# Performance work log

Measured on AMD Instinct MI355X. Metric: run time of the kernel, lower is better.

## Reference

```python
import jax, jax.numpy as jnp
import numpy as np

B, S, IN_F, OUT_F = 8, 2048, 2048, 2048
ORDER, RANK, LEAF = 3, 4, 13  # LEAF = ceil(IN_F ** (1/ORDER))


def setup_inputs() -> dict:
    key = jax.random.key(0)
    k1, k2, k3, k4 = jax.random.split(key, 4)
    inp = jax.random.normal(k1, (B, S, IN_F), dtype=jnp.float32)
    # leaf init ~ uniform(-std, std), std = gain / in_features**(1/order)
    gain = float(np.sqrt(2.0 / (1.0 + 5.0)))  # leaky_relu gain with param=sqrt(5)
    std = gain / (IN_F ** (1.0 / ORDER))
    leaf_tensor = jax.random.uniform(k2, (ORDER, RANK, LEAF, LEAF), dtype=jnp.float32,
                                     minval=-std, maxval=std)
    bound = 1.0 / np.sqrt(IN_F)
    weight = jax.random.uniform(k3, (OUT_F, IN_F), dtype=jnp.float32, minval=-bound, maxval=bound)
    bias = jax.random.uniform(k4, (OUT_F,), dtype=jnp.float32, minval=-bound, maxval=bound)
    return {"input": inp, "leaf_tensor": leaf_tensor, "weight": weight, "bias": bias}


def tensor_product_represent(leaf_tensor, out_dim, in_dim):
    order, rank, leaf, _ = leaf_tensor.shape  # static shapes
    base = leaf_tensor[0]                      # [rank, leaf, leaf]
    dim = leaf
    for i in range(1, order):                  # fixed small structural loop
        # Kronecker step: [r, d, d] x [r, l, l] -> [r, d*l, d*l]
        base = jnp.einsum('abc,ade->abdce', base, leaf_tensor[i])
        dim = dim * leaf
        base = base.reshape(rank, dim, dim)
    base = base.sum(axis=0)                    # [leaf^order, leaf^order]
    return base[:out_dim, :in_dim]


def reference(input, leaf_tensor, weight, bias):
    out_dim, in_dim = weight.shape
    delta = tensor_product_represent(leaf_tensor, out_dim, in_dim)
    w = weight + delta                          # [out, in]
    # F.linear: y = x @ w.T + b
    return jnp.einsum('bsi,oi->bso', input, w) + bias
```

## Files before the change

### kernel.cpp

```cpp
#include <hip/hip_runtime.h>
#include <hip/hip_bf16.h>
#include <stdint.h>

#define MROWS 16384
#define KDIM  2048
#define NDIM  2048
#define LEAFD 13
#define RANKD 4

typedef __bf16 bf16x8 __attribute__((ext_vector_type(8)));
typedef float  f32x4  __attribute__((ext_vector_type(4)));

__global__ void build_w_kernel(const float* __restrict__ weight,
                               const float* __restrict__ leaf,
                               __hip_bfloat16* __restrict__ wbf) {
    __shared__ float ll[3 * RANKD * LEAFD * LEAFD];
    for (int t = threadIdx.x; t < 3 * RANKD * LEAFD * LEAFD; t += blockDim.x)
        ll[t] = leaf[t];
    __syncthreads();
    int idx = blockIdx.x * blockDim.x + threadIdx.x;
    if (idx >= NDIM * KDIM) return;
    int o = idx / KDIM, i = idx % KDIM;
    int o2 = o / 169, o1 = (o / 13) % 13, o0 = o % 13;
    int i2 = i / 169, i1 = (i / 13) % 13, i0 = i % 13;
    float d = 0.f;
#pragma unroll
    for (int r = 0; r < RANKD; ++r) {
        float a = ll[( r            * LEAFD + o2) * LEAFD + i2];
        float b = ll[((RANKD   + r) * LEAFD + o1) * LEAFD + i1];
        float c = ll[((2*RANKD + r) * LEAFD + o0) * LEAFD + i0];
        d += a * b * c;
    }
    wbf[idx] = __float2bfloat16(weight[idx] + d);
}

__global__ void cvt_kernel(const float* __restrict__ x,
                           __hip_bfloat16* __restrict__ xb, int n) {
    long stride = (long)gridDim.x * blockDim.x * 4;
    for (long idx = ((long)blockIdx.x * blockDim.x + threadIdx.x) * 4; idx < n; idx += stride) {
        float4 v = *reinterpret_cast<const float4*>(x + idx);
        __hip_bfloat16 tmp[4];
        tmp[0] = __float2bfloat16(v.x);
        tmp[1] = __float2bfloat16(v.y);
        tmp[2] = __float2bfloat16(v.z);
        tmp[3] = __float2bfloat16(v.w);
        *reinterpret_cast<uint2*>(xb + idx) = *reinterpret_cast<const uint2*>(tmp);
    }
}

#define BM 128
#define BN 128
#define BK 32

__device__ __forceinline__ void gload_lds16(const void* g, void* l) {
    __builtin_amdgcn_global_load_lds((const __attribute__((address_space(1))) void*)g,
                                     (__attribute__((address_space(3))) void*)l,
                                     16, 0, 0);
}

__global__ __launch_bounds__(256) void gemm_kernel(const __hip_bfloat16* __restrict__ A,
                                                   const __hip_bfloat16* __restrict__ Wb,
                                                   const float* __restrict__ bias,
                                                   float* __restrict__ C) {
    __shared__ __hip_bfloat16 sA[BM * BK];
    __shared__ __hip_bfloat16 sB[BN * BK];

    const int bid  = blockIdx.x;
    const int bn   = bid & 15;
    const int bm   = bid >> 4;
    const int tid  = threadIdx.x;
    const int lane = tid & 63;
    const int wid  = tid >> 6;
    const int wr   = wid >> 1;
    const int wc   = wid & 1;

    const size_t arow0 = (size_t)bm * BM;
    const size_t brow0 = (size_t)bn * BN;

    f32x4 acc[4][4];
#pragma unroll
    for (int m = 0; m < 4; ++m)
#pragma unroll
        for (int n = 0; n < 4; ++n)
            acc[m][n] = (f32x4){0.f, 0.f, 0.f, 0.f};

    const int rsel = lane & 15;
    const int ksel = (lane >> 4) * 8;

    for (int kt = 0; kt < KDIM / BK; ++kt) {
        const int k0 = kt * BK;
#pragma unroll
        for (int j = 0; j < 2; ++j) {
            const int c   = (wid * 2 + j) * 64 + lane;
            const int row = c >> 2;
            const int ch  = c & 3;
            const __hip_bfloat16* ga = A  + (arow0 + row) * KDIM + k0 + ch * 8;
            const __hip_bfloat16* gb = Wb + (brow0 + row) * KDIM + k0 + ch * 8;
            gload_lds16(ga, &sA[(wid * 2 + j) * 512]);
            gload_lds16(gb, &sB[(wid * 2 + j) * 512]);
        }
        __syncthreads();

        bf16x8 af[4], bfr[4];
#pragma unroll
        for (int m = 0; m < 4; ++m)
            af[m] = *reinterpret_cast<const bf16x8*>(&sA[(wr * 64 + m * 16 + rsel) * BK + ksel]);
#pragma unroll
        for (int n = 0; n < 4; ++n)
            bfr[n] = *reinterpret_cast<const bf16x8*>(&sB[(wc * 64 + n * 16 + rsel) * BK + ksel]);

#pragma unroll
        for (int m = 0; m < 4; ++m)
#pragma unroll
            for (int n = 0; n < 4; ++n)
                acc[m][n] = __builtin_amdgcn_mfma_f32_16x16x32_bf16(af[m], bfr[n], acc[m][n], 0, 0, 0);

        __syncthreads();
    }

    const int col0 = lane & 15;
    const int r0   = (lane >> 4) * 4;
#pragma unroll
    for (int n = 0; n < 4; ++n) {
        const int cg = bn * BN + wc * 64 + n * 16 + col0;
        const float bv = bias[cg];
#pragma unroll
        for (int m = 0; m < 4; ++m) {
            const size_t rg = arow0 + wr * 64 + m * 16 + r0;
#pragma unroll
            for (int r = 0; r < 4; ++r)
                C[(rg + r) * NDIM + cg] = acc[m][n][r] + bv;
        }
    }
}

__global__ void naive_kernel(const float* __restrict__ x,
                             const float* __restrict__ leaf,
                             const float* __restrict__ W,
                             const float* __restrict__ bias,
                             float* __restrict__ out) {
    long idx = (long)blockIdx.x * blockDim.x + threadIdx.x;
    if (idx >= (long)MROWS * NDIM) return;
    int  o = (int)(idx % NDIM);
    long m = idx / NDIM;
    int o2 = o / 169, o1 = (o / 13) % 13, o0 = o % 13;
    float acc = 0.f;
    for (int i = 0; i < KDIM; ++i) {
        int i2 = i / 169, i1 = (i / 13) % 13, i0 = i % 13;
        float d = 0.f;
#pragma unroll
        for (int r = 0; r < RANKD; ++r)
            d += leaf[( r     * LEAFD + o2) * LEAFD + i2]
               * leaf[((4 + r) * LEAFD + o1) * LEAFD + i1]
               * leaf[((8 + r) * LEAFD + o0) * LEAFD + i0];
        acc += x[m * KDIM + i] * (W[(long)o * KDIM + i] + d);
    }
    out[idx] = acc + bias[o];
}

extern "C" void kernel_launch(void* const* d_in, const int* in_sizes, int n_in,
                              void* d_out, int out_size, void* d_ws, size_t ws_size,
                              hipStream_t stream) {
    const float* x      = (const float*)d_in[0];
    const float* leaf   = (const float*)d_in[1];
    const float* weight = (const float*)d_in[2];
    const float* bias   = (const float*)d_in[3];
    float* out = (float*)d_out;

    const size_t needA = (size_t)MROWS * KDIM * sizeof(__hip_bfloat16);
    const size_t needW = (size_t)NDIM  * KDIM * sizeof(__hip_bfloat16);

    if (ws_size >= needA + needW) {
        __hip_bfloat16* xb = (__hip_bfloat16*)d_ws;
        __hip_bfloat16* wb = (__hip_bfloat16*)((char*)d_ws + needA);
        build_w_kernel<<<(NDIM * KDIM + 255) / 256, 256, 0, stream>>>(weight, leaf, wb);
        cvt_kernel<<<2048, 256, 0, stream>>>(x, xb, MROWS * KDIM);
        gemm_kernel<<<(MROWS / BM) * (NDIM / BN), 256, 0, stream>>>(xb, wb, bias, out);
    } else {
        long total = (long)MROWS * NDIM;
        naive_kernel<<<(int)((total + 255) / 256), 256, 0, stream>>>(x, leaf, weight, bias, out);
    }
}
```

Measured before the change: 248.4 us.

## Replace GEMM with 256x256 double-buffered 8-wave kernel with swizzled LDS

Rewrites the bf16 GEMM to use 256x256 block tiles with 512 threads, a K-step of 64 split into two 32-wide halves, and double-buffered LDS fed by global_load_lds, so the next tile's loads overlap the current MFMAs. LDS addresses are XOR-swizzled to avoid bank conflicts, and block IDs are remapped for better L2 locality. A hand-built schedule of barriers, waitcnts and setprio interleaves the loads with MFMA quarters. The goal is to raise arithmetic intensity and hide memory latency, at the cost of higher register and LDS pressure and a fragile manual schedule.

```diff
diff --git a/kernel.cpp b/kernel.cpp
--- a/kernel.cpp
+++ b/kernel.cpp
@@ -48,85 +48,168 @@
     }
 }
 
-#define BM 128
-#define BN 128
-#define BK 32
-
-__device__ __forceinline__ void gload_lds16(const void* g, void* l) {
+
+__device__ __forceinline__ void gload16(const __hip_bfloat16* g, char* l) {
     __builtin_amdgcn_global_load_lds((const __attribute__((address_space(1))) void*)g,
                                      (__attribute__((address_space(3))) void*)l,
                                      16, 0, 0);
 }
 
-__global__ __launch_bounds__(256) void gemm_kernel(const __hip_bfloat16* __restrict__ A,
-                                                   const __hip_bfloat16* __restrict__ Wb,
-                                                   const float* __restrict__ bias,
-                                                   float* __restrict__ C) {
-    __shared__ __hip_bfloat16 sA[BM * BK];
-    __shared__ __hip_bfloat16 sB[BN * BK];
-
-    const int bid  = blockIdx.x;
-    const int bn   = bid & 15;
-    const int bm   = bid >> 4;
+#define STAGE(base, kb, bufi, slot) do {                                          \
+    gload16((base) + (kb) + gOff0, smemc + (bufi)*65536 + (slot)*16384 + lOff0);  \
+    gload16((base) + (kb) + gOff1, smemc + (bufi)*65536 + (slot)*16384 + lOff1);  \
+} while (0)
+
+#define LOAD_A(mh, kk, bufc)                                                        \
+    af0 = *(const bf16x8*)(smemc + (bufc)*65536 + (kk)*32768 + offA[(mh)*4+0]);     \
+    af1 = *(const bf16x8*)(smemc + (bufc)*65536 + (kk)*32768 + offA[(mh)*4+1]);     \
+    af2 = *(const bf16x8*)(smemc + (bufc)*65536 + (kk)*32768 + offA[(mh)*4+2]);     \
+    af3 = *(const bf16x8*)(smemc + (bufc)*65536 + (kk)*32768 + offA[(mh)*4+3]);
+
+#define LOAD_B(kk, bufc)                                                                    \
+    bf0 = *(const bf16x8*)(smemc + (bufc)*65536 + (kk)*32768 + 16384 + offB[0]);            \
+    bf1 = *(const bf16x8*)(smemc + (bufc)*65536 + (kk)*32768 + 16384 + offB[1]);            \
+    bf2 = *(const bf16x8*)(smemc + (bufc)*65536 + (kk)*32768 + 16384 + offB[2]);            \
+    bf3 = *(const bf16x8*)(smemc + (bufc)*65536 + (kk)*32768 + 16384 + offB[3]);
+
+#define MFMA_Q(mh) do {                                                                   \
+    acc[(mh)*4+0][0] = __builtin_amdgcn_mfma_f32_16x16x32_bf16(af0, bf0, acc[(mh)*4+0][0], 0,0,0); \
+    acc[(mh)*4+1][0] = __builtin_amdgcn_mfma_f32_16x16x32_bf16(af1, bf0, acc[(mh)*4+1][0], 0,0,0); \
+    acc[(mh)*4+2][0] = __builtin_amdgcn_mfma_f32_16x16x32_bf16(af2, bf0, acc[(mh)*4+2][0], 0,0,0); \
+    acc[(mh)*4+3][0] = __builtin_amdgcn_mfma_f32_16x16x32_bf16(af3, bf0, acc[(mh)*4+3][0], 0,0,0); \
+    acc[(mh)*4+0][1] = __builtin_amdgcn_mfma_f32_16x16x32_bf16(af0, bf1, acc[(mh)*4+0][1], 0,0,0); \
+    acc[(mh)*4+1][1] = __builtin_amdgcn_mfma_f32_16x16x32_bf16(af1, bf1, acc[(mh)*4+1][1], 0,0,0); \
+    acc[(mh)*4+2][1] = __builtin_amdgcn_mfma_f32_16x16x32_bf16(af2, bf1, acc[(mh)*4+2][1], 0,0,0); \
+    acc[(mh)*4+3][1] = __builtin_amdgcn_mfma_f32_16x16x32_bf16(af3, bf1, acc[(mh)*4+3][1], 0,0,0); \
+    acc[(mh)*4+0][2] = __builtin_amdgcn_mfma_f32_16x16x32_bf16(af0, bf2, acc[(mh)*4+0][2], 0,0,0); \
+    acc[(mh)*4+1][2] = __builtin_amdgcn_mfma_f32_16x16x32_bf16(af1, bf2, acc[(mh)*4+1][2], 0,0,0); \
+    acc[(mh)*4+2][2] = __builtin_amdgcn_mfma_f32_16x16x32_bf16(af2, bf2, acc[(mh)*4+2][2], 0,0,0); \
+    acc[(mh)*4+3][2] = __builtin_amdgcn_mfma_f32_16x16x32_bf16(af3, bf2, acc[(mh)*4+3][2], 0,0,0); \
+    acc[(mh)*4+0][3] = __builtin_amdgcn_mfma_f32_16x16x32_bf16(af0, bf3, acc[(mh)*4+0][3], 0,0,0); \
+    acc[(mh)*4+1][3] = __builtin_amdgcn_mfma_f32_16x16x32_bf16(af1, bf3, acc[(mh)*4+1][3], 0,0,0); \
+    acc[(mh)*4+2][3] = __builtin_amdgcn_mfma_f32_16x16x32_bf16(af2, bf3, acc[(mh)*4+2][3], 0,0,0); \
+    acc[(mh)*4+3][3] = __builtin_amdgcn_mfma_f32_16x16x32_bf16(af3, bf3, acc[(mh)*4+3][3], 0,0,0); \
+} while (0)
+
+#define BARRIER_IN do {                                     \
+    __builtin_amdgcn_sched_barrier(0);                      \
+    __builtin_amdgcn_s_barrier();                           \
+    asm volatile("s_waitcnt lgkmcnt(0)" ::: "memory");      \
+    __builtin_amdgcn_sched_barrier(0);                      \
+    __builtin_amdgcn_s_setprio(1);                          \
+} while (0)
+
+#define BARRIER_OUT do {                                    \
+    __builtin_amdgcn_s_setprio(0);                          \
+    __builtin_amdgcn_sched_barrier(0);                      \
+    __builtin_amdgcn_s_barrier();                           \
+    __builtin_amdgcn_sched_barrier(0);                      \
+} while (0)
+
+#define WAIT4 asm volatile("s_waitcnt vmcnt(4)" ::: "memory")
+#define WAIT0 asm volatile("s_waitcnt vmcnt(0)" ::: "memory")
+#define WNONE do {} while (0)
+
+#define KTILE(t, bufc, S0, S1, S2, S3, W3) do {                     \
+                                                  \
+    LOAD_B(0, bufc); LOAD_A(0, 0, bufc);                            \
+    if (S0) STAGE(Abase, ((t)+1)*64+32, (bufc)^1, 2);               \
+    BARRIER_IN; MFMA_Q(0); BARRIER_OUT;                             \
+                                                  \
+    LOAD_A(1, 0, bufc);                                             \
+    if (S1) STAGE(Bbase, ((t)+1)*64+32, (bufc)^1, 3);               \
+    BARRIER_IN; MFMA_Q(1); BARRIER_OUT;                             \
+                                                  \
+    LOAD_B(1, bufc); LOAD_A(0, 1, bufc);                            \
+    if (S2) STAGE(Abase, ((t)+2)*64, (bufc), 0);                    \
+    BARRIER_IN; MFMA_Q(0); BARRIER_OUT;                             \
+                                                  \
+    LOAD_A(1, 1, bufc);                                             \
+    if (S3) STAGE(Bbase, ((t)+2)*64, (bufc), 1);                    \
+    W3;                                                             \
+    BARRIER_IN; MFMA_Q(1); BARRIER_OUT;                             \
+} while (0)
+
+__global__ __launch_bounds__(512, 2) void gemm8_kernel(const __hip_bfloat16* __restrict__ A,
+                                                       const __hip_bfloat16* __restrict__ Wb,
+                                                       const float* __restrict__ bias,
+                                                       float* __restrict__ C) {
+    __shared__ __align__(16) __hip_bfloat16 smem[2][4][8192];
+    char* smemc = (char*)&smem[0][0][0];
+
     const int tid  = threadIdx.x;
     const int lane = tid & 63;
     const int wid  = tid >> 6;
-    const int wr   = wid >> 1;
-    const int wc   = wid & 1;
-
-    const size_t arow0 = (size_t)bm * BM;
-    const size_t brow0 = (size_t)bn * BN;
-
-    f32x4 acc[4][4];
-#pragma unroll
-    for (int m = 0; m < 4; ++m)
+    const int wr   = wid >> 2;
+    const int wc   = wid & 3;
+
+    const int bid = blockIdx.x;
+    const int swz = (bid & 7) * 64 + (bid >> 3);
+    const int bn  = swz >> 6;
+    const int bm  = swz & 63;
+
+    const __hip_bfloat16* Abase = A  + (size_t)bm * 256 * KDIM;
+    const __hip_bfloat16* Bbase = Wb + (size_t)bn * 256 * KDIM;
+
+    const int c0  = wid * 64 + lane;
+    const int c1  = 512 + wid * 64 + lane;
+    const int cs0 = c0 ^ ((c0 >> 3) & 7);
+    const int cs1 = c1 ^ ((c1 >> 3) & 7);
+    const int gOff0 = (cs0 >> 2) * KDIM + (cs0 & 3) * 8;
+    const int gOff1 = (cs1 >> 2) * KDIM + (cs1 & 3) * 8;
+    const int lOff0 = wid * 1024;
+    const int lOff1 = 8192 + wid * 1024;
+
+    const int rsel = lane & 15;
+    const int kby  = (lane >> 4) * 16;
+    int offA[8], offB[4];
+#pragma unroll
+    for (int m = 0; m < 8; ++m) {
+        int a = (wr * 128 + m * 16 + rsel) * 64 + kby;
+        offA[m] = a ^ (((a >> 7) & 7) << 4);
+    }
+#pragma unroll
+    for (int n = 0; n < 4; ++n) {
+        int a = (wc * 64 + n * 16 + rsel) * 64 + kby;
+        offB[n] = a ^ (((a >> 7) & 7) << 4);
+    }
+
+    f32x4 acc[8][4];
+#pragma unroll
+    for (int m = 0; m < 8; ++m)
 #pragma unroll
         for (int n = 0; n < 4; ++n)
             acc[m][n] = (f32x4){0.f, 0.f, 0.f, 0.f};
 
-    const int rsel = lane & 15;
-    const int ksel = (lane >> 4) * 8;
-
-    for (int kt = 0; kt < KDIM / BK; ++kt) {
-        const int k0 = kt * BK;
-#pragma unroll
-        for (int j = 0; j < 2; ++j) {
-            const int c   = (wid * 2 + j) * 64 + lane;
-            const int row = c >> 2;
-            const int ch  = c & 3;
-            const __hip_bfloat16* ga = A  + (arow0 + row) * KDIM + k0 + ch * 8;
-            const __hip_bfloat16* gb = Wb + (brow0 + row) * KDIM + k0 + ch * 8;
-            gload_lds16(ga, &sA[(wid * 2 + j) * 512]);
-            gload_lds16(gb, &sB[(wid * 2 + j) * 512]);
-        }
-        __syncthreads();
-
-        bf16x8 af[4], bfr[4];
-#pragma unroll
-        for (int m = 0; m < 4; ++m)
-            af[m] = *reinterpret_cast<const bf16x8*>(&sA[(wr * 64 + m * 16 + rsel) * BK + ksel]);
-#pragma unroll
-        for (int n = 0; n < 4; ++n)
-            bfr[n] = *reinterpret_cast<const bf16x8*>(&sB[(wc * 64 + n * 16 + rsel) * BK + ksel]);
-
-#pragma unroll
-        for (int m = 0; m < 4; ++m)
-#pragma unroll
-            for (int n = 0; n < 4; ++n)
-                acc[m][n] = __builtin_amdgcn_mfma_f32_16x16x32_bf16(af[m], bfr[n], acc[m][n], 0, 0, 0);
-
-        __syncthreads();
-    }
+    bf16x8 af0, af1, af2, af3, bf0, bf1, bf2, bf3;
+
+    STAGE(Abase,  0, 0, 0);
+    STAGE(Bbase,  0, 0, 1);
+    STAGE(Abase, 32, 0, 2);
+    STAGE(Bbase, 32, 0, 3);
+    STAGE(Abase, 64, 1, 0);
+    STAGE(Bbase, 64, 1, 1);
+    WAIT4;
+    __builtin_amdgcn_sched_barrier(0);
+    __builtin_amdgcn_s_barrier();
+    __builtin_amdgcn_sched_barrier(0);
+
+    for (int tt = 0; tt < 30; tt += 2) {
+        KTILE(tt,     0, 1, 1, 1, 1, WAIT4);
+        KTILE(tt + 1, 1, 1, 1, 1, 1, WAIT4);
+    }
+    KTILE(30, 0, 1, 1, 0, 0, WAIT0);
+    KTILE(31, 1, 0, 0, 0, 0, WNONE);
 
     const int col0 = lane & 15;
     const int r0   = (lane >> 4) * 4;
 #pragma unroll
     for (int n = 0; n < 4; ++n) {
-        const int cg = bn * BN + wc * 64 + n * 16 + col0;
+        const int cg = bn * 256 + wc * 64 + n * 16 + col0;
         const float bv = bias[cg];
 #pragma unroll
-        for (int m = 0; m < 4; ++m) {
-            const size_t rg = arow0 + wr * 64 + m * 16 + r0;
+        for (int m = 0; m < 8; ++m) {
+            const size_t rg = (size_t)bm * 256 + wr * 128 + m * 16 + r0;
 #pragma unroll
             for (int r = 0; r < 4; ++r)
                 C[(rg + r) * NDIM + cg] = acc[m][n][r] + bv;
@@ -175,7 +258,7 @@
         __hip_bfloat16* wb = (__hip_bfloat16*)((char*)d_ws + needA);
         build_w_kernel<<<(NDIM * KDIM + 255) / 256, 256, 0, stream>>>(weight, leaf, wb);
         cvt_kernel<<<2048, 256, 0, stream>>>(x, xb, MROWS * KDIM);
-        gemm_kernel<<<(MROWS / BM) * (NDIM / BN), 256, 0, stream>>>(xb, wb, bias, out);
+        gemm8_kernel<<<(MROWS / 256) * (NDIM / 256), 512, 0, stream>>>(xb, wb, bias, out);
     } else {
         long total = (long)MROWS * NDIM;
         naive_kernel<<<(int)((total + 255) / 256), 256, 0, stream>>>(x, leaf, weight, bias, out);
```

Result: faster. 208.3 us (-16.1%).

## Rewrite GEMM with triple-buffered LDS pipeline, XOR swizzle, and 128x256 tiles

Applied to the files above, without the earlier changes.

Replaces the single-buffered 128x128 GEMM with a 512-thread 128x256-tile kernel. It uses a three-stage global_load_lds ring with explicit vmcnt waits and a single barrier per k-step, XOR-swizzled LDS addressing to avoid bank conflicts, and a block-index swizzle for L2 reuse. It also raises MFMA priority via s_setprio and widens the fp32-to-bf16 conversion to 8 elements per thread. This aims to hide load latency and remove the double-syncthreads stalls, at the cost of more LDS per block and fragile hand-tuned waitcnt logic.

```diff
diff --git a/kernel.cpp b/kernel.cpp
--- a/kernel.cpp
+++ b/kernel.cpp
@@ -36,46 +36,127 @@
 
 __global__ void cvt_kernel(const float* __restrict__ x,
                            __hip_bfloat16* __restrict__ xb, int n) {
-    long stride = (long)gridDim.x * blockDim.x * 4;
-    for (long idx = ((long)blockIdx.x * blockDim.x + threadIdx.x) * 4; idx < n; idx += stride) {
-        float4 v = *reinterpret_cast<const float4*>(x + idx);
-        __hip_bfloat16 tmp[4];
-        tmp[0] = __float2bfloat16(v.x);
-        tmp[1] = __float2bfloat16(v.y);
-        tmp[2] = __float2bfloat16(v.z);
-        tmp[3] = __float2bfloat16(v.w);
-        *reinterpret_cast<uint2*>(xb + idx) = *reinterpret_cast<const uint2*>(tmp);
-    }
-}
-
-#define BM 128
-#define BN 128
-#define BK 32
-
-__device__ __forceinline__ void gload_lds16(const void* g, void* l) {
+    long stride = (long)gridDim.x * blockDim.x * 8;
+    for (long idx = ((long)blockIdx.x * blockDim.x + threadIdx.x) * 8; idx < n; idx += stride) {
+        float4 v0 = *reinterpret_cast<const float4*>(x + idx);
+        float4 v1 = *reinterpret_cast<const float4*>(x + idx + 4);
+        __hip_bfloat16 tmp[8];
+        tmp[0] = __float2bfloat16(v0.x); tmp[1] = __float2bfloat16(v0.y);
+        tmp[2] = __float2bfloat16(v0.z); tmp[3] = __float2bfloat16(v0.w);
+        tmp[4] = __float2bfloat16(v1.x); tmp[5] = __float2bfloat16(v1.y);
+        tmp[6] = __float2bfloat16(v1.z); tmp[7] = __float2bfloat16(v1.w);
+        *reinterpret_cast<uint4*>(xb + idx) = *reinterpret_cast<const uint4*>(tmp);
+    }
+}
+
+
+__device__ __forceinline__ void gload16(const __hip_bfloat16* g, char* l) {
     __builtin_amdgcn_global_load_lds((const __attribute__((address_space(1))) void*)g,
                                      (__attribute__((address_space(3))) void*)l,
                                      16, 0, 0);
 }
 
-__global__ __launch_bounds__(256) void gemm_kernel(const __hip_bfloat16* __restrict__ A,
-                                                   const __hip_bfloat16* __restrict__ Wb,
-                                                   const float* __restrict__ bias,
-                                                   float* __restrict__ C) {
-    __shared__ __hip_bfloat16 sA[BM * BK];
-    __shared__ __hip_bfloat16 sB[BN * BK];
-
-    const int bid  = blockIdx.x;
-    const int bn   = bid & 15;
-    const int bm   = bid >> 4;
+#define RD(off) (*(const bf16x8*)(smemc + (off)))
+
+#define MFMA16 do {                                                                 \
+    acc[0][0] = __builtin_amdgcn_mfma_f32_16x16x32_bf16(af0, bf0, acc[0][0],0,0,0); \
+    acc[1][0] = __builtin_amdgcn_mfma_f32_16x16x32_bf16(af1, bf0, acc[1][0],0,0,0); \
+    acc[2][0] = __builtin_amdgcn_mfma_f32_16x16x32_bf16(af2, bf0, acc[2][0],0,0,0); \
+    acc[3][0] = __builtin_amdgcn_mfma_f32_16x16x32_bf16(af3, bf0, acc[3][0],0,0,0); \
+    acc[0][1] = __builtin_amdgcn_mfma_f32_16x16x32_bf16(af0, bf1, acc[0][1],0,0,0); \
+    acc[1][1] = __builtin_amdgcn_mfma_f32_16x16x32_bf16(af1, bf1, acc[1][1],0,0,0); \
+    acc[2][1] = __builtin_amdgcn_mfma_f32_16x16x32_bf16(af2, bf1, acc[2][1],0,0,0); \
+    acc[3][1] = __builtin_amdgcn_mfma_f32_16x16x32_bf16(af3, bf1, acc[3][1],0,0,0); \
+    acc[0][2] = __builtin_amdgcn_mfma_f32_16x16x32_bf16(af0, bf2, acc[0][2],0,0,0); \
+    acc[1][2] = __builtin_amdgcn_mfma_f32_16x16x32_bf16(af1, bf2, acc[1][2],0,0,0); \
+    acc[2][2] = __builtin_amdgcn_mfma_f32_16x16x32_bf16(af2, bf2, acc[2][2],0,0,0); \
+    acc[3][2] = __builtin_amdgcn_mfma_f32_16x16x32_bf16(af3, bf2, acc[3][2],0,0,0); \
+    acc[0][3] = __builtin_amdgcn_mfma_f32_16x16x32_bf16(af0, bf3, acc[0][3],0,0,0); \
+    acc[1][3] = __builtin_amdgcn_mfma_f32_16x16x32_bf16(af1, bf3, acc[1][3],0,0,0); \
+    acc[2][3] = __builtin_amdgcn_mfma_f32_16x16x32_bf16(af2, bf3, acc[2][3],0,0,0); \
+    acc[3][3] = __builtin_amdgcn_mfma_f32_16x16x32_bf16(af3, bf3, acc[3][3],0,0,0); \
+} while (0)
+
+#define W3 asm volatile("s_waitcnt vmcnt(3)" ::: "memory")
+#define W0 asm volatile("s_waitcnt vmcnt(0)" ::: "memory")
+
+#define KT(t, BC, BS, SG, WT) do {                                              \
+    af0 = RD((BC)*24576 + offA0);                                               \
+    af1 = RD((BC)*24576 + offA0 + 1024);                                        \
+    af2 = RD((BC)*24576 + offA0 + 2048);                                        \
+    af3 = RD((BC)*24576 + offA0 + 3072);                                        \
+    bf0 = RD((BC)*24576 + 8192 + offB0);                                        \
+    bf1 = RD((BC)*24576 + 8192 + offB0 + 1024);                                 \
+    bf2 = RD((BC)*24576 + 8192 + offB0 + 2048);                                 \
+    bf3 = RD((BC)*24576 + 8192 + offB0 + 3072);                                 \
+    if (SG) {                                                                   \
+        gload16(Abase + ((t)+2)*32 + gA,  smemc + (BS)*24576 + lA);             \
+        gload16(Bbase + ((t)+2)*32 + gB0, smemc + (BS)*24576 + 8192 + lB0);     \
+        gload16(Bbase + ((t)+2)*32 + gB1, smemc + (BS)*24576 + 8192 + lB1);     \
+    }                                                                           \
+    __builtin_amdgcn_s_setprio(1);                                              \
+    MFMA16;                                                                     \
+    __builtin_amdgcn_s_setprio(0);                                              \
+    WT;                                                                         \
+    __builtin_amdgcn_s_barrier();                                               \
+} while (0)
+
+#define KT_LAST(BC) do {                                                        \
+    af0 = RD((BC)*24576 + offA0);                                               \
+    af1 = RD((BC)*24576 + offA0 + 1024);                                        \
+    af2 = RD((BC)*24576 + offA0 + 2048);                                        \
+    af3 = RD((BC)*24576 + offA0 + 3072);                                        \
+    bf0 = RD((BC)*24576 + 8192 + offB0);                                        \
+    bf1 = RD((BC)*24576 + 8192 + offB0 + 1024);                                 \
+    bf2 = RD((BC)*24576 + 8192 + offB0 + 2048);                                 \
+    bf3 = RD((BC)*24576 + 8192 + offB0 + 3072);                                 \
+    __builtin_amdgcn_s_setprio(1);                                              \
+    MFMA16;                                                                     \
+    __builtin_amdgcn_s_setprio(0);                                              \
+} while (0)
+
+__global__ __launch_bounds__(512, 4) void gemm10_kernel(const __hip_bfloat16* __restrict__ A,
+                                                        const __hip_bfloat16* __restrict__ Wb,
+                                                        const float* __restrict__ bias,
+                                                        float* __restrict__ C) {
+    __shared__ __align__(16) char smem_raw[3 * 24576];
+    char* smemc = smem_raw;
+
     const int tid  = threadIdx.x;
     const int lane = tid & 63;
     const int wid  = tid >> 6;
-    const int wr   = wid >> 1;
-    const int wc   = wid & 1;
-
-    const size_t arow0 = (size_t)bm * BM;
-    const size_t brow0 = (size_t)bn * BN;
+    const int wr   = wid >> 2;
+    const int wc   = wid & 3;
+
+    const int bid = blockIdx.x;
+    const int swz = (bid & 7) * 128 + (bid >> 3);
+    const int bn  = swz >> 7;
+    const int bm  = swz & 127;
+
+    const __hip_bfloat16* Abase = A  + (size_t)bm * 128 * KDIM;
+    const __hip_bfloat16* Bbase = Wb + (size_t)bn * 256 * KDIM;
+
+    int gA, gB0, gB1;
+    {
+        const int cA = tid;
+        const int sA = cA ^ ((cA >> 3) & 7);
+        gA = (sA >> 2) * KDIM + (sA & 3) * 8;
+        const int c0 = tid;
+        const int s0 = c0 ^ ((c0 >> 3) & 7);
+        gB0 = (s0 >> 2) * KDIM + (s0 & 3) * 8;
+        const int c1 = tid + 512;
+        const int s1 = c1 ^ ((c1 >> 3) & 7);
+        gB1 = (s1 >> 2) * KDIM + (s1 & 3) * 8;
+    }
+    const int lA  = wid * 1024;
+    const int lB0 = wid * 1024;
+    const int lB1 = 8192 + wid * 1024;
+
+    const int rsel = lane & 15;
+    const int kq   = lane >> 4;
+    const int xmask = ((rsel >> 1) & 7) << 4;
+    const int offA0 = (((wr * 64 + rsel) * 64) + kq * 16) ^ xmask;
+    const int offB0 = (((wc * 64 + rsel) * 64) + kq * 16) ^ xmask;
 
     f32x4 acc[4][4];
 #pragma unroll
@@ -84,49 +165,35 @@
         for (int n = 0; n < 4; ++n)
             acc[m][n] = (f32x4){0.f, 0.f, 0.f, 0.f};
 
-    const int rsel = lane & 15;
-    const int ksel = (lane >> 4) * 8;
-
-    for (int kt = 0; kt < KDIM / BK; ++kt) {
-        const int k0 = kt * BK;
-#pragma unroll
-        for (int j = 0; j < 2; ++j) {
-            const int c   = (wid * 2 + j) * 64 + lane;
-            const int row = c >> 2;
-            const int ch  = c & 3;
-            const __hip_bfloat16* ga = A  + (arow0 + row) * KDIM + k0 + ch * 8;
-            const __hip_bfloat16* gb = Wb + (brow0 + row) * KDIM + k0 + ch * 8;
-            gload_lds16(ga, &sA[(wid * 2 + j) * 512]);
-            gload_lds16(gb, &sB[(wid * 2 + j) * 512]);
-        }
-        __syncthreads();
-
-        bf16x8 af[4], bfr[4];
-#pragma unroll
-        for (int m = 0; m < 4; ++m)
-            af[m] = *reinterpret_cast<const bf16x8*>(&sA[(wr * 64 + m * 16 + rsel) * BK + ksel]);
-#pragma unroll
-        for (int n = 0; n < 4; ++n)
-            bfr[n] = *reinterpret_cast<const bf16x8*>(&sB[(wc * 64 + n * 16 + rsel) * BK + ksel]);
-
-#pragma unroll
-        for (int m = 0; m < 4; ++m)
-#pragma unroll
-            for (int n = 0; n < 4; ++n)
-                acc[m][n] = __builtin_amdgcn_mfma_f32_16x16x32_bf16(af[m], bfr[n], acc[m][n], 0, 0, 0);
-
-        __syncthreads();
-    }
-
-    const int col0 = lane & 15;
-    const int r0   = (lane >> 4) * 4;
+    bf16x8 af0, af1, af2, af3, bf0, bf1, bf2, bf3;
+
+    gload16(Abase +  0 + gA,  smemc + lA);
+    gload16(Bbase +  0 + gB0, smemc + 8192 + lB0);
+    gload16(Bbase +  0 + gB1, smemc + 8192 + lB1);
+    gload16(Abase + 32 + gA,  smemc + 24576 + lA);
+    gload16(Bbase + 32 + gB0, smemc + 24576 + 8192 + lB0);
+    gload16(Bbase + 32 + gB1, smemc + 24576 + 8192 + lB1);
+    W3;
+    __builtin_amdgcn_s_barrier();
+
+    for (int t = 0; t < 60; t += 3) {
+        KT(t,     0, 2, 1, W3);
+        KT(t + 1, 1, 0, 1, W3);
+        KT(t + 2, 2, 1, 1, W3);
+    }
+    KT(60, 0, 2, 1, W3);
+    KT(61, 1, 0, 1, W3);
+    KT(62, 2, 1, 0, W0);
+    KT_LAST(0);
+
+    const int r0 = kq * 4;
 #pragma unroll
     for (int n = 0; n < 4; ++n) {
-        const int cg = bn * BN + wc * 64 + n * 16 + col0;
+        const int cg = bn * 256 + wc * 64 + n * 16 + rsel;
         const float bv = bias[cg];
 #pragma unroll
         for (int m = 0; m < 4; ++m) {
-            const size_t rg = arow0 + wr * 64 + m * 16 + r0;
+            const size_t rg = (size_t)bm * 128 + wr * 64 + m * 16 + r0;
 #pragma unroll
             for (int r = 0; r < 4; ++r)
                 C[(rg + r) * NDIM + cg] = acc[m][n][r] + bv;
@@ -175,7 +242,7 @@
         __hip_bfloat16* wb = (__hip_bfloat16*)((char*)d_ws + needA);
         build_w_kernel<<<(NDIM * KDIM + 255) / 256, 256, 0, stream>>>(weight, leaf, wb);
         cvt_kernel<<<2048, 256, 0, stream>>>(x, xb, MROWS * KDIM);
-        gemm_kernel<<<(MROWS / BM) * (NDIM / BN), 256, 0, stream>>>(xb, wb, bias, out);
+        gemm10_kernel<<<(MROWS / 128) * (NDIM / 256), 512, 0, stream>>>(xb, wb, bias, out);
     } else {
         long total = (long)MROWS * NDIM;
         naive_kernel<<<(int)((total + 255) / 256), 256, 0, stream>>>(x, leaf, weight, bias, out);
```

After: 218.6 us. 1.14x faster.
